# Optimization experiments

Measured on AMD Instinct MI355X. Metric: run time of the kernel, lower is better.

Reference implementation:

```python
import jax, jax.numpy as jnp
import numpy as np

P = 10          # num_patches
EPS = 1e-20
ALPHAS = dict(stretch=1.0, E=1.0, G=1.0, skew=1.0, total_area=1.0, total_area_mult=1.0)
ALPHA_MC = 1.0
ALPHA_DISTORT = 1.0


def setup_inputs() -> dict:
    key = jax.random.key(0)
    k1, k2, k3, k4 = jax.random.split(key, 4)
    B, N, M = 8, 8192, 2500
    pc_gt = jax.random.normal(k1, (B, N, 3), dtype=jnp.float32)
    pc_pred = jax.random.normal(k2, (B, M, 3), dtype=jnp.float32)
    # first fundamental form (E, F, G); ensure E*G - F^2 > 0 so sqrt is smooth
    u = jax.random.uniform(k3, (B, M, 3), dtype=jnp.float32)
    fff = u * 0.5 + jnp.array([1.0, 0.0, 1.0], dtype=jnp.float32)
    A_gt = jax.random.uniform(k4, (B,), dtype=jnp.float32)
    return {"pc_gt": pc_gt, "pc_pred": pc_pred, "fff": fff, "A_gt": A_gt}


def _forward(pc_gt, pc_pred, fff, A_gt):
    B, M, _ = pc_pred.shape
    spp = M // P

    # ---- Chamfer distance via dense (B, M, N) distance matrix + argmin ----
    diff = pc_pred[:, :, None, :] - pc_gt[:, None, :, :]          # (B, M, N, 3)
    distm = jnp.sqrt(jnp.sum(diff * diff, axis=3))                # (B, M, N)
    inds_p2gt = jnp.argmin(distm, axis=2)                         # (B, M)
    inds_gt2p = jnp.argmin(distm, axis=1)                         # (B, N)
    pc_gt_reg = jnp.take_along_axis(pc_gt, inds_p2gt[..., None], axis=1)   # (B, M, 3)
    pc_p_reg = jnp.take_along_axis(pc_pred, inds_gt2p[..., None], axis=1)  # (B, N, 3)
    d_p2gt = jnp.sum((pc_pred - pc_gt_reg) ** 2, axis=2)
    d_gt2p = jnp.sum((pc_gt - pc_p_reg) ** 2, axis=2)
    L_chd = d_p2gt.mean() + d_gt2p.mean()

    # ---- FFF-based losses ----
    EFG = jnp.transpose(fff.reshape(B, P, spp, 3), (3, 0, 1, 2))  # (3, B, P, spp)
    E, F, G = EFG[0], EFG[1], EFG[2]

    # metric consistency between consecutive frame pairs
    Eh = E.reshape(B // 2, 2, P, spp)
    Fh = F.reshape(B // 2, 2, P, spp)
    Gh = G.reshape(B // 2, 2, P, spp)
    L_mc = ((Eh[:, 0] - Eh[:, 1]) ** 2
            + 2.0 * (Fh[:, 0] - Fh[:, 1]) ** 2
            + (Gh[:, 0] - Gh[:, 1]) ** 2).mean()

    # scaled isometry (collapse) losses
    A2 = jnp.maximum(E * G - F * F, 0.0)                          # (B, P, spp)
    A = jnp.sqrt(A2)
    inv = 1.0 / (A2 + EPS)
    L_stretch = (((E - G) ** 2) * inv).mean() * ALPHAS['stretch']
    L_E = (((E - E.mean()) ** 2) * inv).mean() * ALPHAS['E']
    L_G = (((G - G.mean()) ** 2) * inv).mean() * ALPHAS['G']
    L_F = ((F * F) * inv).mean() * ALPHAS['skew']

    # overlap / total-area loss
    A_tot = A.mean(axis=2).sum(axis=1)                            # (B,)
    L_olap = (jnp.maximum(0.0, A_tot - A_gt * ALPHAS['total_area_mult']) ** 2).mean() * ALPHAS['total_area']

    loss_sciso = L_F + L_E + L_G + L_stretch + L_olap
    loss_tot = L_chd + ALPHA_MC * L_mc + ALPHA_DISTORT * loss_sciso
    return loss_tot


def reference(pc_gt, pc_pred, fff, A_gt):
    return _forward(pc_gt, pc_pred, fff, A_gt)
```

## Files before the change

kernel.cpp:

```cpp
#include <hip/hip_runtime.h>

#define B_   8
#define N_   8192
#define M_   2500
#define SPP_ 250
#define EPS_ 1e-20f
#define BIGF 1e30f

#define NB_P2GT 320
#define NB_GT2P 256
#define NB_FFF  79
#define NB_K1   (NB_P2GT + NB_GT2P + NB_FFF)

#define NB_RG2P 256
#define NB_RP2  79
#define NB_K2   (NB_RG2P + NB_RP2)

#define WS_P2GT 0
#define WS_GT2P 160000
#define WS_ACC  291072
#define WS_RED  291092
#define WS_CNT  291427
#define A_E    0
#define A_G    1
#define A_MC   2
#define A_ST   3
#define A_F2I  4
#define A_E2I  5
#define A_EI   6
#define A_G2I  7
#define A_GI   8
#define A_I    9
#define A_AB   10
#define RO_G2P 0
#define RO_P2  256

typedef __attribute__((ext_vector_type(8))) short short8_t;
typedef __attribute__((ext_vector_type(4))) float float4_t;

__device__ __forceinline__ unsigned pack_bf2(float lo, float hi) {
    unsigned a = __float_as_uint(lo);
    unsigned b = __float_as_uint(hi);
    a = (a + 0x7FFFu + ((a >> 16) & 1u)) >> 16;
    b = (b + 0x7FFFu + ((b >> 16) & 1u)) & 0xFFFF0000u;
    return a | b;
}
__device__ __forceinline__ short bf16s(float x) {
    unsigned a = __float_as_uint(x);
    return (short)((a + 0x7FFFu + ((a >> 16) & 1u)) >> 16);
}
__device__ __forceinline__ float wave_sum64(float v) {
    #pragma unroll
    for (int o = 32; o > 0; o >>= 1) v += __shfl_down(v, o, 64);
    return v;
}
__device__ __forceinline__ float block_sum256(float v, volatile float* red4) {
    v = wave_sum64(v);
    int wid = threadIdx.x >> 6, lane = threadIdx.x & 63;
    if (lane == 0) red4[wid] = v;
    __syncthreads();
    float r = 0.f;
    if (threadIdx.x == 0) r = red4[0] + red4[1] + red4[2] + red4[3];
    __syncthreads();
    return r;
}
__device__ __forceinline__ void min4(float4_t& c, const float4_t d) {
    c.x = fminf(c.x, d.x); c.y = fminf(c.y, d.y);
    c.z = fminf(c.z, d.z); c.w = fminf(c.w, d.w);
}
__device__ __forceinline__ void quad_min4(float4_t& c) {
    #pragma unroll
    for (int m = 1; m < 16; m <<= 1) {
        c.x = fminf(c.x, __shfl_xor(c.x, m, 64));
        c.y = fminf(c.y, __shfl_xor(c.y, m, 64));
        c.z = fminf(c.z, __shfl_xor(c.z, m, 64));
        c.w = fminf(c.w, __shfl_xor(c.w, m, 64));
    }
}

__global__ void __launch_bounds__(256, 2) k1_main(
        const float* __restrict__ gt, const float* __restrict__ pred,
        const float* __restrict__ fff, float* __restrict__ ws) {
    __shared__ uint4 spts[1280];
    __shared__ __align__(16) float saux[516];
    const int bid = blockIdx.x;
    const int tid = threadIdx.x;
    const int lane = tid & 63;
    const int w    = tid >> 6;
    const int quad = lane >> 4;
    const int l15  = lane & 15;
    float* acc = ws + WS_ACC;

    if (bid == 0 && tid == 0) ((unsigned*)(ws + WS_CNT))[0] = 0u;

    if (bid < NB_P2GT + NB_GT2P) {
        const bool is_p2gt = bid < NB_P2GT;
        int b, mblk, z, ntiles, blim, alim;
        const float* apts; const float* bpts; float* dst;
        if (is_p2gt) {
            z = bid / 40; int rem = bid % 40;
            b = rem / 5;  mblk = rem % 5;
            apts = pred + (size_t)b * M_ * 3;
            bpts = gt + ((size_t)b * N_ + (size_t)z * 1024) * 3;
            ntiles = 64; blim = 1024; alim = M_;
            dst = ws + WS_P2GT + (size_t)z * 20000 + b * M_;
        } else {
            int r = bid - NB_P2GT;
            z = r >> 7; int rem = r & 127;
            b = rem >> 4; mblk = rem & 15;
            apts = gt + (size_t)b * N_ * 3;
            bpts = pred + ((size_t)b * M_ + (size_t)z * 1280) * 3;
            ntiles = 80; blim = M_ - z * 1280; alim = N_;
            dst = ws + WS_GT2P + (size_t)z * 65536 + b * N_;
        }
        const int abase = mblk * 512;
        const int nstage = ntiles * 16;

        for (int i = tid; i < nstage; i += 256) {
            float x = 0.f, y = 0.f, zc = 0.f, n2 = BIGF;
            if (i < blim) {
                x = bpts[i * 3 + 0]; y = bpts[i * 3 + 1]; zc = bpts[i * 3 + 2];
                n2 = x * x + y * y + zc * zc;
            }
            uint4 q;
            q.x = pack_bf2(-2.f * x, -2.f * y);
            q.y = pack_bf2(-2.f * zc, n2);
            q.z = q.x; q.w = q.y;
            spts[i] = q;
        }

        short8_t af[8];
        #pragma unroll
        for (int t = 0; t < 8; ++t) af[t] = (short8_t){0,0,0,0,0,0,0,0};
        if (lane < 16) {
            #pragma unroll
            for (int t = 0; t < 8; ++t) {
                int m = abase + w * 128 + t * 16 + l15;
                int c = m < alim ? m : alim - 1;
                float x = apts[c*3+0], y = apts[c*3+1], zc = apts[c*3+2];
                af[t][0] = bf16s(x); af[t][1] = bf16s(y); af[t][2] = bf16s(zc);
                af[t][3] = (short)0x3F80;
                saux[w * 128 + t * 16 + l15] = x*x + y*y + zc*zc;
            }
        }
        __syncthreads();

        const float4_t* bp = (const float4_t*)saux;
        float4_t bias[8], c[8];
        #pragma unroll
        for (int t = 0; t < 8; ++t) {
            bias[t] = bp[w * 32 + t * 4 + quad];
            c[t] = (float4_t){BIGF, BIGF, BIGF, BIGF};
        }

        const uint4* bptr = spts + l15;
        #pragma unroll 2
        for (int i = 0; i < ntiles; ++i) {
            short8_t bf = __builtin_bit_cast(short8_t, bptr[i * 16]);
            #pragma unroll
            for (int t = 0; t < 8; ++t) {
                float4_t d = __builtin_amdgcn_mfma_f32_16x16x32_bf16(
                                 af[t], bf, bias[t], 0, 0, 0);
                min4(c[t], d);
            }
        }
        #pragma unroll
        for (int t = 0; t < 8; ++t) {
            quad_min4(c[t]);
            c[t].x = fmaxf(c[t].x, 0.f); c[t].y = fmaxf(c[t].y, 0.f);
            c[t].z = fmaxf(c[t].z, 0.f); c[t].w = fmaxf(c[t].w, 0.f);
        }
        if (l15 == 0) {
            #pragma unroll
            for (int t = 0; t < 8; ++t) {
                int m0 = abase + w * 128 + t * 16 + quad * 4;
                if (m0 < alim)
                    *(float4_t*)(dst + m0) = c[t];
            }
        }
    } else {
        const int kb = bid - NB_P2GT - NB_GT2P;
        const int i  = kb * 256 + tid;
        volatile float* red4 = saux + 512;
        float* sA = saux;
        if (tid < B_) sA[tid] = 0.f;
        __syncthreads();

        float vE=0.f,vG=0.f,vMC=0.f,vST=0.f,vF2=0.f,vE2=0.f,vEI=0.f,
              vG2=0.f,vGI=0.f,vI=0.f;
        if (i < B_ * M_) {
            const int b = i / M_;
            const int m = i - b * M_;
            const float* f = fff + (size_t)i * 3;
            float E = f[0], F = f[1], G = f[2];
            float A2  = fmaxf(E * G - F * F, 0.f);
            float inv = 1.f / (A2 + EPS_);
            vE = E; vG = G;
            vST = (E - G) * (E - G) * inv;
            vF2 = F * F * inv;
            vE2 = E * E * inv; vEI = E * inv;
            vG2 = G * G * inv; vGI = G * inv;
            vI  = inv;
            atomicAdd(&sA[b], sqrtf(A2));
            if ((b & 1) == 0) {
                const float* f2 = fff + ((size_t)(b + 1) * M_ + m) * 3;
                float dE = E - f2[0], dF = F - f2[1], dG = G - f2[2];
                vMC = dE * dE + 2.f * dF * dF + dG * dG;
            }
        }
        float r;
        r = block_sum256(vE,  red4); if (tid==0) atomicAdd(&acc[A_E],   r);
        r = block_sum256(vG,  red4); if (tid==0) atomicAdd(&acc[A_G],   r);
        r = block_sum256(vMC, red4); if (tid==0) atomicAdd(&acc[A_MC],  r);
        r = block_sum256(vST, red4); if (tid==0) atomicAdd(&acc[A_ST],  r);
        r = block_sum256(vF2, red4); if (tid==0) atomicAdd(&acc[A_F2I], r);
        r = block_sum256(vE2, red4); if (tid==0) atomicAdd(&acc[A_E2I], r);
        r = block_sum256(vEI, red4); if (tid==0) atomicAdd(&acc[A_EI],  r);
        r = block_sum256(vG2, red4); if (tid==0) atomicAdd(&acc[A_G2I], r);
        r = block_sum256(vGI, red4); if (tid==0) atomicAdd(&acc[A_GI],  r);
        r = block_sum256(vI,  red4); if (tid==0) atomicAdd(&acc[A_I],   r);
        __syncthreads();
        if (tid < B_ && sA[tid] != 0.f) atomicAdd(&acc[A_AB + tid], sA[tid]);
    }
}

__global__ void __launch_bounds__(256) k2_reduce(
        const float* __restrict__ fff, const float* __restrict__ A_gt,
        float* __restrict__ ws, float* __restrict__ out) {
    __shared__ float red4[4];
    const int bid = blockIdx.x;
    const int tid = threadIdx.x;
    float* redp = ws + WS_RED;
    float* acc  = ws + WS_ACC;

    if (bid < NB_RG2P) {
        const int o = bid * 256 + tid;
        const float* src = ws + WS_GT2P + o;
        float m = fminf(src[0], src[65536]);
        float r = block_sum256(m, red4);
        if (tid == 0) redp[RO_G2P + bid] = r;
    } else {
        const int kb = bid - NB_RG2P;
        const int o = kb * 256 + tid;
        float s = 0.f;
        if (o < 20000) {
            const float* src = ws + WS_P2GT + o;
            float m = src[0];
            #pragma unroll
            for (int zz = 1; zz < 8; ++zz) m = fminf(m, src[zz * 20000]);
            s = m;
        }
        float r = block_sum256(s, red4);
        if (tid == 0) redp[RO_P2 + kb] = r;
    }

    __syncthreads();
    if (tid == 0) __threadfence();
    __syncthreads();
    __shared__ unsigned old_s;
    if (tid == 0)
        old_s = __hip_atomic_fetch_add((unsigned*)(ws + WS_CNT), 1u,
                                       __ATOMIC_ACQ_REL, __HIP_MEMORY_SCOPE_AGENT);
    __syncthreads();
    if (old_s == (unsigned)(NB_K2 - 1)) {
        float v;
        v = redp[RO_G2P + tid];
        float sGT2P = block_sum256(v, red4);
        v = (tid < 79) ? redp[RO_P2 + tid] : 0.f;
        float sP2GT = block_sum256(v, red4);
        if (tid == 0) {
            float a[18];
            #pragma unroll
            for (int k = 0; k < 18; ++k)
                a[k] = __hip_atomic_load(&acc[k], __ATOMIC_RELAXED,
                                         __HIP_MEMORY_SCOPE_AGENT);
            const float inv20k = 1.f / 20000.f;
            float mE = a[A_E] * inv20k, mG = a[A_G] * inv20k;
            float L_E = (a[A_E2I] - 2.f*mE*a[A_EI] + mE*mE*a[A_I]) * inv20k;
            float L_G = (a[A_G2I] - 2.f*mG*a[A_GI] + mG*mG*a[A_I]) * inv20k;
            float L_sc = L_E + L_G + (a[A_ST] + a[A_F2I]) * inv20k;
            float L_mc = a[A_MC] * (1.f / 10000.f);
            float L_chd = sP2GT * inv20k + sGT2P * (1.f / 65536.f);
            float L_olap = 0.f;
            #pragma unroll
            for (int b = 0; b < B_; ++b) {
                float At = a[A_AB + b] * (1.f / (float)SPP_);
                float d  = fmaxf(0.f, At - A_gt[b]);
                L_olap += d * d;
            }
            L_olap *= (1.f / (float)B_);
            out[0] = L_chd + L_mc + L_sc + L_olap;
        }
    }
}

extern "C" void kernel_launch(void* const* d_in, const int* in_sizes, int n_in,
                              void* d_out, int out_size, void* d_ws, size_t ws_size,
                              hipStream_t stream) {
    const float* pc_gt   = (const float*)d_in[0];
    const float* pc_pred = (const float*)d_in[1];
    const float* fff     = (const float*)d_in[2];
    const float* A_gt    = (const float*)d_in[3];
    float* ws  = (float*)d_ws;
    float* out = (float*)d_out;

    hipMemsetAsync(ws + WS_ACC, 0, 20 * sizeof(float), stream);
    k1_main  <<<NB_K1, 256, 0, stream>>>(pc_gt, pc_pred, fff, ws);
    k2_reduce<<<NB_K2, 256, 0, stream>>>(fff, A_gt, ws, out);
}
```

Before: 96.52 us.

## Compute both Chamfer directions from one shared distance-tile pass

Removes the separate gt-to-pred block set and instead takes column-wise minima of the same MFMA distance tiles used for the pred-to-gt minima. Each block writes per-gt-point partial minima through shared memory into a workspace laid out by mblk, and the second kernel reduces over five partials instead of two. This halves the matrix work but adds per-tile in-lane min reductions, two cross-lane shuffles, shared-memory stores and extra LDS, which may lower occupancy.

Measured after the change: 104.0 us. +7.8%, slower.

```diff
diff --git a/kernel.cpp b/kernel.cpp
--- a/kernel.cpp
+++ b/kernel.cpp
@@ -7,10 +7,9 @@
 #define EPS_ 1e-20f
 #define BIGF 1e30f
 
-#define NB_P2GT 320
-#define NB_GT2P 256
+#define NB_CH   320
 #define NB_FFF  79
-#define NB_K1   (NB_P2GT + NB_GT2P + NB_FFF)
+#define NB_K1   (NB_CH + NB_FFF)
 
 #define NB_RG2P 256
 #define NB_RP2  79
@@ -18,9 +17,9 @@
 
 #define WS_P2GT 0
 #define WS_GT2P 160000
-#define WS_ACC  291072
-#define WS_RED  291092
-#define WS_CNT  291427
+#define WS_ACC  487680
+#define WS_RED  487700
+#define WS_CNT  488035
 #define A_E    0
 #define A_G    1
 #define A_MC   2
@@ -81,8 +80,9 @@
 __global__ void __launch_bounds__(256, 2) k1_main(
         const float* __restrict__ gt, const float* __restrict__ pred,
         const float* __restrict__ fff, float* __restrict__ ws) {
-    __shared__ uint4 spts[1280];
+    __shared__ uint4 spts[1024];
     __shared__ __align__(16) float saux[516];
+    __shared__ float scol[4][1024];
     const int bid = blockIdx.x;
     const int tid = threadIdx.x;
     const int lane = tid & 63;
@@ -93,35 +93,22 @@
 
     if (bid == 0 && tid == 0) ((unsigned*)(ws + WS_CNT))[0] = 0u;
 
-    if (bid < NB_P2GT + NB_GT2P) {
-        const bool is_p2gt = bid < NB_P2GT;
-        int b, mblk, z, ntiles, blim, alim;
-        const float* apts; const float* bpts; float* dst;
-        if (is_p2gt) {
-            z = bid / 40; int rem = bid % 40;
-            b = rem / 5;  mblk = rem % 5;
-            apts = pred + (size_t)b * M_ * 3;
-            bpts = gt + ((size_t)b * N_ + (size_t)z * 1024) * 3;
-            ntiles = 64; blim = 1024; alim = M_;
-            dst = ws + WS_P2GT + (size_t)z * 20000 + b * M_;
-        } else {
-            int r = bid - NB_P2GT;
-            z = r >> 7; int rem = r & 127;
-            b = rem >> 4; mblk = rem & 15;
-            apts = gt + (size_t)b * N_ * 3;
-            bpts = pred + ((size_t)b * M_ + (size_t)z * 1280) * 3;
-            ntiles = 80; blim = M_ - z * 1280; alim = N_;
-            dst = ws + WS_GT2P + (size_t)z * 65536 + b * N_;
-        }
+    if (bid < NB_CH) {
+        const int z = bid / 40;
+        const int rem = bid % 40;
+        const int b = rem / 5;
+        const int mblk = rem % 5;
+        const float* apts = pred + (size_t)b * M_ * 3;
+        const float* bpts = gt + ((size_t)b * N_ + (size_t)z * 1024) * 3;
+        const int alim = M_;
         const int abase = mblk * 512;
-        const int nstage = ntiles * 16;
-
-        for (int i = tid; i < nstage; i += 256) {
-            float x = 0.f, y = 0.f, zc = 0.f, n2 = BIGF;
-            if (i < blim) {
-                x = bpts[i * 3 + 0]; y = bpts[i * 3 + 1]; zc = bpts[i * 3 + 2];
-                n2 = x * x + y * y + zc * zc;
-            }
+        float* dstR = ws + WS_P2GT + (size_t)z * 20000 + b * M_;
+        float* dstC = ws + WS_GT2P + (size_t)mblk * 65536 + b * N_ + z * 1024;
+
+        for (int i = tid; i < 1024; i += 256) {
+            const float* q3 = bpts + i * 3;
+            float x = q3[0], y = q3[1], zc = q3[2];
+            float n2 = x * x + y * y + zc * zc;
             uint4 q;
             q.x = pack_bf2(-2.f * x, -2.f * y);
             q.y = pack_bf2(-2.f * zc, n2);
@@ -155,15 +142,23 @@
 
         const uint4* bptr = spts + l15;
         #pragma unroll 2
-        for (int i = 0; i < ntiles; ++i) {
+        for (int i = 0; i < 64; ++i) {
             short8_t bf = __builtin_bit_cast(short8_t, bptr[i * 16]);
+            float cmA = BIGF, cmB = BIGF;
             #pragma unroll
             for (int t = 0; t < 8; ++t) {
                 float4_t d = __builtin_amdgcn_mfma_f32_16x16x32_bf16(
                                  af[t], bf, bias[t], 0, 0, 0);
                 min4(c[t], d);
-            }
-        }
+                float m0 = fminf(fminf(d.x, d.y), fminf(d.z, d.w));
+                if (t & 1) cmB = fminf(cmB, m0); else cmA = fminf(cmA, m0);
+            }
+            float cm = fminf(cmA, cmB);
+            cm = fminf(cm, __shfl_xor(cm, 16, 64));
+            cm = fminf(cm, __shfl_xor(cm, 32, 64));
+            if (lane < 16) scol[w][i * 16 + l15] = cm;
+        }
+
         #pragma unroll
         for (int t = 0; t < 8; ++t) {
             quad_min4(c[t]);
@@ -175,11 +170,19 @@
             for (int t = 0; t < 8; ++t) {
                 int m0 = abase + w * 128 + t * 16 + quad * 4;
                 if (m0 < alim)
-                    *(float4_t*)(dst + m0) = c[t];
-            }
+                    *(float4_t*)(dstR + m0) = c[t];
+            }
+        }
+
+        __syncthreads();
+        #pragma unroll
+        for (int j = tid; j < 1024; j += 256) {
+            float v = fminf(fminf(scol[0][j], scol[1][j]),
+                            fminf(scol[2][j], scol[3][j]));
+            dstC[j] = fmaxf(v, 0.f);
         }
     } else {
-        const int kb = bid - NB_P2GT - NB_GT2P;
+        const int kb = bid - NB_CH;
         const int i  = kb * 256 + tid;
         volatile float* red4 = saux + 512;
         float* sA = saux;
@@ -236,7 +239,9 @@
     if (bid < NB_RG2P) {
         const int o = bid * 256 + tid;
         const float* src = ws + WS_GT2P + o;
-        float m = fminf(src[0], src[65536]);
+        float m = src[0];
+        #pragma unroll
+        for (int zz = 1; zz < 5; ++zz) m = fminf(m, src[zz * 65536]);
         float r = block_sum256(m, red4);
         if (tid == 0) redp[RO_G2P + bid] = r;
     } else {
```
